# Optimization experiments

Measured on AMD Instinct MI355X. Metric: run time of the kernel, lower is better.

## Reference

```python
import jax, jax.numpy as jnp
import numpy as np

V, C, D = 131072, 65536, 128
E_NEG, E_CON = 131072, 524288
L, B = 3, 32


def setup_inputs() -> dict:
    key = jax.random.key(0)
    ks = jax.random.split(key, 16)
    s = 1.0 / np.sqrt(D)
    return {
        "x_var": jax.random.normal(ks[0], (V, D), jnp.float32),
        "x_con": jax.random.normal(ks[1], (C, D), jnp.float32),
        "W_src": jax.random.normal(ks[2], (L, 3, D, D), jnp.float32) * s,
        "W_dst": jax.random.normal(ks[3], (L, 3, D, D), jnp.float32) * s,
        "att_src": jax.random.normal(ks[4], (L, 3, D), jnp.float32) * s,
        "att_dst": jax.random.normal(ks[5], (L, 3, D), jnp.float32) * s,
        "bias": jnp.zeros((L, 3, D), jnp.float32),
        "mlp_w1": jax.random.normal(ks[6], (D, D), jnp.float32) * s,
        "mlp_b1": jnp.zeros((D,), jnp.float32),
        "mlp_w2": jax.random.normal(ks[7], (D, 1), jnp.float32) * s,
        "mlp_b2": jnp.zeros((1,), jnp.float32),
        "edge_neg_src": jax.random.randint(ks[8], (E_NEG,), 0, V, jnp.int32),
        "edge_neg_dst": jax.random.randint(ks[9], (E_NEG,), 0, V, jnp.int32),
        "edge_con_src": jax.random.randint(ks[10], (E_CON,), 0, V, jnp.int32),
        "edge_con_dst": jax.random.randint(ks[11], (E_CON,), 0, C, jnp.int32),
        "batch_var": jnp.sort(jax.random.randint(ks[12], (V,), 0, B, jnp.int32)),
    }


def _gat(xs, xd, src, dst, Ws, Wd, a_s, a_d, b, n_dst):
    """PyG GATConv (heads=1, add_self_loops=False) for one bipartite relation."""
    hs = xs @ Ws                                    # [Ns, D]
    hd = xd @ Wd                                    # [Nd, D]
    es = hs @ a_s                                   # [Ns]
    ed = hd @ a_d                                   # [Nd]
    e = jax.nn.leaky_relu(es[src] + ed[dst], negative_slope=0.2)  # [E]
    m = jax.ops.segment_max(e, dst, num_segments=n_dst)
    m = jnp.where(jnp.isfinite(m), m, 0.0)
    ex = jnp.exp(e - m[dst])
    den = jax.ops.segment_sum(ex, dst, num_segments=n_dst)
    alpha = ex / (den[dst] + 1e-16)                 # per-destination softmax
    out = jax.ops.segment_sum(hs[src] * alpha[:, None], dst, num_segments=n_dst)
    return out + b


def reference(x_var, x_con, W_src, W_dst, att_src, att_dst, bias,
              mlp_w1, mlp_b1, mlp_w2, mlp_b2,
              edge_neg_src, edge_neg_dst, edge_con_src, edge_con_dst, batch_var):
    xv, xc = x_var, x_con
    n_layers = W_src.shape[0]
    for l in range(n_layers):
        # relation 0: variable -is_negation_of-> variable
        v_neg = _gat(xv, xv, edge_neg_src, edge_neg_dst,
                     W_src[l, 0], W_dst[l, 0], att_src[l, 0], att_dst[l, 0], bias[l, 0], V)
        # relation 2: constraint -rev_connected_to-> variable (reverse edges)
        v_rev = _gat(xc, xv, edge_con_dst, edge_con_src,
                     W_src[l, 2], W_dst[l, 2], att_src[l, 2], att_dst[l, 2], bias[l, 2], V)
        # relation 1: variable -connected_to-> constraint
        c_new = _gat(xv, xc, edge_con_src, edge_con_dst,
                     W_src[l, 1], W_dst[l, 1], att_src[l, 1], att_dst[l, 1], bias[l, 1], C)
        # HeteroConv aggr='sum', then relu (dropout is identity in eval)
        xv = jax.nn.relu(v_neg + v_rev)
        xc = jax.nn.relu(c_new)
    # global_mean_pool over variable nodes per graph
    cnt = jax.ops.segment_sum(jnp.ones((V,), xv.dtype), batch_var, num_segments=B)
    pooled = jax.ops.segment_sum(xv, batch_var, num_segments=B) / jnp.maximum(cnt, 1.0)[:, None]
    # vote MLP: Linear -> relu -> Linear
    h = jax.nn.relu(pooled @ mlp_w1 + mlp_b1)
    return h @ mlp_w2 + mlp_b2
```

## Files before the change

### kernel.cpp

```cpp
#include <hip/hip_runtime.h>
#include <hip/hip_bf16.h>
#include <cstdint>
#include <cstddef>

#define D 128

typedef __hip_bfloat16 bf16;
typedef __attribute__((ext_vector_type(8))) short short8v;
typedef __attribute__((ext_vector_type(4))) float f32x4;

__device__ inline float ld1(const float* p) { return *p; }
__device__ inline float ld1(const bf16* p) { return __bfloat162float(*p); }
__device__ inline float2 ld2(const float* p) { return *(const float2*)p; }
__device__ inline float2 ld2(const bf16* p) {
  __hip_bfloat162 v = *(const __hip_bfloat162*)p;
  float2 r; r.x = __bfloat162float(v.x); r.y = __bfloat162float(v.y); return r;
}
__device__ inline void st2(float* p, float a, float b) {
  float2 v; v.x = a; v.y = b; *(float2*)p = v;
}
__device__ inline void st2(bf16* p, float a, float b) {
  __hip_bfloat162 v; v.x = __float2bfloat16(a); v.y = __float2bfloat16(b);
  *(__hip_bfloat162*)p = v;
}

__device__ inline short f2bf(float x) {
  uint32_t u = __builtin_bit_cast(uint32_t, x);
  uint32_t r = (u + 0x7FFFu + ((u >> 16) & 1u)) >> 16;
  return (short)(uint16_t)r;
}
__device__ inline float bf2f(short s) {
  uint32_t u = ((uint32_t)(uint16_t)s) << 16;
  return __builtin_bit_cast(float, u);
}

__device__ inline f32x4 mfma16(short8v a, short8v b, f32x4 c) {
  return __builtin_amdgcn_mfma_f32_16x16x32_bf16(a, b, c, 0, 0, 0);
}

__device__ __forceinline__ void load8(const float* p, float* v) {
  float4 a = *(const float4*)p;
  float4 b = *(const float4*)(p + 4);
  v[0] = a.x; v[1] = a.y; v[2] = a.z; v[3] = a.w;
  v[4] = b.x; v[5] = b.y; v[6] = b.z; v[7] = b.w;
}

__global__ void compute_u_kernel(const float* __restrict__ Wsrc, const float* __restrict__ Wdst,
                                 const float* __restrict__ asrc, const float* __restrict__ adst,
                                 float* __restrict__ u) {
  int lr = blockIdx.x;
  int side = blockIdx.y;
  int k = threadIdx.x;
  const float* W = (side == 0 ? Wsrc : Wdst) + ((size_t)lr * D + k) * D;
  const float* a = (side == 0 ? asrc : adst) + (size_t)lr * D;
  float s = 0.f;
  for (int j = 0; j < D; ++j) s += W[j] * a[j];
  u[((size_t)lr * 2 + side) * D + k] = s;
}

__global__ void wsplit_kernel(const float* __restrict__ Wsrc,
                              short* __restrict__ WhT, short* __restrict__ WlT) {
  int lr = blockIdx.x;
  const float* W = Wsrc + (size_t)lr * D * D;
  short* wh = WhT + (size_t)lr * D * D;
  short* wl = WlT + (size_t)lr * D * D;
  for (int i = threadIdx.x; i < D * D; i += blockDim.x) {
    int k = i >> 7, c = i & 127;
    float w = W[i];
    short h = f2bf(w);
    short l = f2bf(w - bf2f(h));
    wh[c * D + k] = h;
    wl[c * D + k] = l;
  }
}

__global__ void usplit_kernel(const float* __restrict__ u,
                              short* __restrict__ uh, short* __restrict__ ul, int L) {
  int l = blockIdx.x;
  int j = blockIdx.y;
  int k = threadIdx.x;
  int rel, side;
  switch (j) {
    case 0: rel = 0; side = 0; break;
    case 1: rel = 0; side = 1; break;
    case 2: rel = 1; side = 0; break;
    case 3: rel = 2; side = 1; break;
    case 4: rel = 2; side = 0; break;
    default: rel = 1; side = 1; break;
  }
  float w = u[(((size_t)l * 3 + rel) * 2 + side) * D + k];
  short h = f2bf(w);
  uh[((size_t)l * 6 + j) * D + k] = h;
  ul[((size_t)l * 6 + j) * D + k] = f2bf(w - bf2f(h));
}

__global__ void count_kernel(const int* __restrict__ dst, int* __restrict__ cnt, int E) {
  int i = blockIdx.x * blockDim.x + threadIdx.x;
  if (i < E) atomicAdd(&cnt[dst[i]], 1);
}

__global__ void count2_kernel(const int* __restrict__ csrc, const int* __restrict__ cdst,
                              int* __restrict__ cnt_bycon, int* __restrict__ cnt_byvar, int E) {
  int i = blockIdx.x * blockDim.x + threadIdx.x;
  if (i < E) {
    atomicAdd(&cnt_bycon[cdst[i]], 1);
    atomicAdd(&cnt_byvar[csrc[i]], 1);
  }
}

__global__ void bsum3_kernel(const int* __restrict__ c0, const int* __restrict__ c1,
                             const int* __restrict__ c2, int* __restrict__ bsums,
                             int n0, int n1, int n2, int pb0, int pb1, int pb2) {
  __shared__ int red[256];
  int y = blockIdx.y;
  const int* cnt = (y == 0) ? c0 : (y == 1) ? c1 : c2;
  int n  = (y == 0) ? n0 : (y == 1) ? n1 : n2;
  int pb = (y == 0) ? pb0 : (y == 1) ? pb1 : pb2;
  int b = blockIdx.x, t = threadIdx.x;
  int base = b * pb;
  if (base >= n) return;
  int end = base + pb; if (end > n) end = n;
  int s = 0;
  for (int i = base + t; i < end; i += 256) s += cnt[i];
  red[t] = s;
  __syncthreads();
  #pragma unroll
  for (int off = 128; off; off >>= 1) {
    if (t < off) red[t] += red[t + off];
    __syncthreads();
  }
  if (t == 0) bsums[y * 1024 + b] = red[0];
}

__global__ void bscan3_kernel(int* __restrict__ bsums,
                              int* __restrict__ t0, int* __restrict__ t1, int* __restrict__ t2) {
  __shared__ int sh[1024];
  int y = blockIdx.x, t = threadIdx.x;
  int* bs = bsums + y * 1024;
  int v = bs[t];
  sh[t] = v;
  __syncthreads();
  for (int off = 1; off < 1024; off <<= 1) {
    int u = (t >= off) ? sh[t - off] : 0;
    __syncthreads();
    sh[t] += u;
    __syncthreads();
  }
  bs[t] = sh[t] - v;
  if (t == 1023) {
    int* tot = (y == 0) ? t0 : (y == 1) ? t1 : t2;
    *tot = sh[1023];
  }
}

__global__ void scanfill3_kernel(const int* __restrict__ c0, const int* __restrict__ c1,
                                 const int* __restrict__ c2, const int* __restrict__ bsums,
                                 int* __restrict__ rp0, int* __restrict__ rp1, int* __restrict__ rp2,
                                 int* __restrict__ cu0, int* __restrict__ cu1, int* __restrict__ cu2,
                                 int n0, int n1, int n2, int pb0, int pb1, int pb2) {
  __shared__ int sh[256];
  int y = blockIdx.y;
  const int* cnt = (y == 0) ? c0 : (y == 1) ? c1 : c2;
  int* rowptr    = (y == 0) ? rp0 : (y == 1) ? rp1 : rp2;
  int* cursor    = (y == 0) ? cu0 : (y == 1) ? cu1 : cu2;
  int n  = (y == 0) ? n0 : (y == 1) ? n1 : n2;
  int pb = (y == 0) ? pb0 : (y == 1) ? pb1 : pb2;
  int b = blockIdx.x, t = threadIdx.x;
  int base = b * pb;
  if (base >= n) return;
  int end = base + pb; if (end > n) end = n;
  int run = bsums[y * 1024 + b];
  for (int tile = base; tile < end; tile += 256) {
    int i = tile + t;
    int c = (i < end) ? cnt[i] : 0;
    __syncthreads();
    sh[t] = c;
    __syncthreads();
    for (int off = 1; off < 256; off <<= 1) {
      int u = (t >= off) ? sh[t - off] : 0;
      __syncthreads();
      sh[t] += u;
      __syncthreads();
    }
    int excl = sh[t] - c;
    if (i < end) {
      rowptr[i] = run + excl;
      cursor[i] = run + excl;
    }
    run += sh[255];
  }
}

__global__ void fill_kernel(const int* __restrict__ dst, const int* __restrict__ src,
                            int* __restrict__ cursor, int* __restrict__ col, int E) {
  int i = blockIdx.x * blockDim.x + threadIdx.x;
  if (i < E) {
    int p = atomicAdd(&cursor[dst[i]], 1);
    col[p] = src[i];
  }
}

__global__ void fill2_kernel(const int* __restrict__ csrc, const int* __restrict__ cdst,
                             int* __restrict__ cur_bycon, int* __restrict__ cur_byvar,
                             int* __restrict__ col_bycon, int* __restrict__ col_byvar, int E) {
  int i = blockIdx.x * blockDim.x + threadIdx.x;
  if (i < E) {
    int s = csrc[i], d = cdst[i];
    int p = atomicAdd(&cur_bycon[d], 1);
    col_bycon[p] = s;
    int q = atomicAdd(&cur_byvar[s], 1);
    col_byvar[q] = d;
  }
}

template<typename Tin>
__global__ __launch_bounds__(256) void mm3r_kernel(
    const Tin* __restrict__ Xv, const Tin* __restrict__ Xc,
    const short* __restrict__ wh0, const short* __restrict__ wl0,
    const short* __restrict__ wh1, const short* __restrict__ wl1,
    const short* __restrict__ wh2, const short* __restrict__ wl2,
    const short* __restrict__ uah, const short* __restrict__ ual,
    bf16* __restrict__ H0, bf16* __restrict__ H1, bf16* __restrict__ H2,
    float* __restrict__ es0, float* __restrict__ ed0,
    float* __restrict__ es1, float* __restrict__ ed2,
    float* __restrict__ es2, float* __restrict__ ed1,
    int V, int C, int b0, int b1, int b2) {
  int bid = blockIdx.x;
  const Tin* X; const short* wh; const short* wl; bf16* H;
  int nrows, lb, nblk, nu;
  const short* auh; const short* aul;
  float *o0, *o1, *o2, *o3;
  if (bid < b0) {
    X = Xv; wh = wh0; wl = wl0; H = H0; nrows = V; lb = bid; nblk = b0;
    nu = 4; auh = uah; aul = ual;
    o0 = es0; o1 = ed0; o2 = es1; o3 = ed2;
  } else if (bid < b1) {
    X = Xv; wh = wh1; wl = wl1; H = H1; nrows = V; lb = bid - b0; nblk = b1 - b0;
    nu = 0; auh = nullptr; aul = nullptr; o0 = o1 = o2 = o3 = nullptr;
  } else {
    X = Xc; wh = wh2; wl = wl2; H = H2; nrows = C; lb = bid - b1; nblk = b2 - b1;
    nu = 2; auh = uah + 4 * D; aul = ual + 4 * D;
    o0 = es2; o1 = ed1; o2 = o3 = nullptr;
  }
  int nchunks = (nrows + 15) >> 4;
  int tid = threadIdx.x;
  int cp = tid >> 6, lane = tid & 63;
  int c15 = lane & 15, q = lane >> 4;

  short8v Wh_[2][4], Wl_[2][4];
  #pragma unroll
  for (int t = 0; t < 2; ++t) {
    #pragma unroll
    for (int ks = 0; ks < 4; ++ks) {
      int o = (cp * 32 + t * 16 + c15) * D + ks * 32 + q * 8;
      Wh_[t][ks] = *(const short8v*)&wh[o];
      Wl_[t][ks] = *(const short8v*)&wl[o];
    }
  }
  bool doaug = (cp == 0) && (nu > 0);
  short8v Uh_[4], Ul_[4];
  if (doaug) {
    #pragma unroll
    for (int ks = 0; ks < 4; ++ks) {
      if (c15 < nu) {
        int o = c15 * D + ks * 32 + q * 8;
        Uh_[ks] = *(const short8v*)&auh[o];
        Ul_[ks] = *(const short8v*)&aul[o];
      } else {
        Uh_[ks] = (short8v){0, 0, 0, 0, 0, 0, 0, 0};
        Ul_[ks] = (short8v){0, 0, 0, 0, 0, 0, 0, 0};
      }
    }
  }

  for (int ch = lb; ch < nchunks; ch += nblk) {
    int row = ch * 16 + c15;
    bool valid = row < nrows;
    if (!valid) row = nrows - 1;
    const Tin* xp = X + (size_t)row * D + q * 8;
    f32x4 a0 = (f32x4){0.f, 0.f, 0.f, 0.f};
    f32x4 a1 = (f32x4){0.f, 0.f, 0.f, 0.f};
    f32x4 a2 = (f32x4){0.f, 0.f, 0.f, 0.f};
    if constexpr (sizeof(Tin) == 2) {
      short8v xf[4];
      #pragma unroll
      for (int ks = 0; ks < 4; ++ks)
        xf[ks] = *(const short8v*)((const short*)xp + ks * 32);
      #pragma unroll
      for (int ks = 0; ks < 4; ++ks) {
        a0 = mfma16(Wh_[0][ks], xf[ks], a0);
        a0 = mfma16(Wl_[0][ks], xf[ks], a0);
        a1 = mfma16(Wh_[1][ks], xf[ks], a1);
        a1 = mfma16(Wl_[1][ks], xf[ks], a1);
        if (doaug) {
          a2 = mfma16(Uh_[ks], xf[ks], a2);
          a2 = mfma16(Ul_[ks], xf[ks], a2);
        }
      }
    } else {
      short8v xh[4], xl[4];
      #pragma unroll
      for (int ks = 0; ks < 4; ++ks) {
        float v[8];
        load8((const float*)xp + ks * 32, v);
        #pragma unroll
        for (int j = 0; j < 8; ++j) {
          short hj = f2bf(v[j]);
          xh[ks][j] = hj;
          xl[ks][j] = f2bf(v[j] - bf2f(hj));
        }
      }
      #pragma unroll
      for (int ks = 0; ks < 4; ++ks) {
        a0 = mfma16(Wh_[0][ks], xh[ks], a0);
        a0 = mfma16(Wl_[0][ks], xh[ks], a0);
        a0 = mfma16(Wh_[0][ks], xl[ks], a0);
        a1 = mfma16(Wh_[1][ks], xh[ks], a1);
        a1 = mfma16(Wl_[1][ks], xh[ks], a1);
        a1 = mfma16(Wh_[1][ks], xl[ks], a1);
        if (doaug) {
          a2 = mfma16(Uh_[ks], xh[ks], a2);
          a2 = mfma16(Ul_[ks], xh[ks], a2);
          a2 = mfma16(Uh_[ks], xl[ks], a2);
        }
      }
    }
    if (valid) {
      short4 s0, s1;
      s0.x = f2bf(a0[0]); s0.y = f2bf(a0[1]); s0.z = f2bf(a0[2]); s0.w = f2bf(a0[3]);
      s1.x = f2bf(a1[0]); s1.y = f2bf(a1[1]); s1.z = f2bf(a1[2]); s1.w = f2bf(a1[3]);
      size_t hb = (size_t)row * D + cp * 32 + q * 4;
      *(short4*)((short*)H + hb) = s0;
      *(short4*)((short*)H + hb + 16) = s1;
      if (doaug && q == 0) {
        o0[row] = a2[0];
        o1[row] = a2[1];
        if (nu == 4) { o2[row] = a2[2]; o3[row] = a2[3]; }
      }
    }
  }
}

__device__ __forceinline__ void alpha_rel(const int* __restrict__ rp, const int* __restrict__ col,
                                          const float* __restrict__ es, float edst,
                                          int gw, int lane, int2* __restrict__ edata) {
  int p0 = rp[gw];
  int deg = rp[gw + 1] - p0;
  if (deg <= 0) return;
  if (deg <= 64) {
    int s = 0; float e = -3.0e38f;
    if (lane < deg) {
      s = col[p0 + lane];
      float t = es[s] + edst;
      e = t > 0.f ? t : 0.2f * t;
    }
    float m = e;
    #pragma unroll
    for (int off = 32; off; off >>= 1) m = fmaxf(m, __shfl_xor(m, off));
    float ex = (lane < deg) ? __expf(e - m) : 0.f;
    float den = ex;
    #pragma unroll
    for (int off = 32; off; off >>= 1) den += __shfl_xor(den, off);
    float al = ex / (den + 1e-16f);
    if (lane < deg) {
      int2 v; v.x = s; v.y = __builtin_bit_cast(int, al);
      edata[p0 + lane] = v;
    }
  } else {
    float m = -3.0e38f;
    for (int j = lane; j < deg; j += 64) {
      int s = col[p0 + j];
      float t = es[s] + edst;
      t = t > 0.f ? t : 0.2f * t;
      m = fmaxf(m, t);
    }
    #pragma unroll
    for (int off = 32; off; off >>= 1) m = fmaxf(m, __shfl_xor(m, off));
    float den = 0.f;
    for (int j = lane; j < deg; j += 64) {
      int s = col[p0 + j];
      float t = es[s] + edst;
      t = t > 0.f ? t : 0.2f * t;
      den += __expf(t - m);
    }
    #pragma unroll
    for (int off = 32; off; off >>= 1) den += __shfl_xor(den, off);
    float inv = 1.f / (den + 1e-16f);
    for (int j = lane; j < deg; j += 64) {
      int s = col[p0 + j];
      float t = es[s] + edst;
      t = t > 0.f ? t : 0.2f * t;
      int2 v; v.x = s; v.y = __builtin_bit_cast(int, __expf(t - m) * inv);
      edata[p0 + j] = v;
    }
  }
}

__global__ void alpha_all_kernel(const int* __restrict__ rp0, const int* __restrict__ col0,
                                 const float* __restrict__ es0, const float* __restrict__ ed0,
                                 int2* __restrict__ eda0,
                                 const int* __restrict__ rp2, const int* __restrict__ col2,
                                 const float* __restrict__ es2, const float* __restrict__ ed2,
                                 int2* __restrict__ eda2,
                                 const int* __restrict__ rp1, const int* __restrict__ col1,
                                 const float* __restrict__ es1, const float* __restrict__ ed1,
                                 int2* __restrict__ eda1,
                                 int V, int C) {
  int gw = (int)(((size_t)blockIdx.x * blockDim.x + threadIdx.x) >> 6);
  int lane = threadIdx.x & 63;
  if (gw < V) {
    alpha_rel(rp0, col0, es0, ed0[gw], gw, lane, eda0);
    alpha_rel(rp2, col2, es2, ed2[gw], gw, lane, eda2);
  } else if (gw < V + C) {
    int g = gw - V;
    alpha_rel(rp1, col1, es1, ed1[g], g, lane, eda1);
  }
}

__device__ __forceinline__ void agg_rel(const int2* __restrict__ edata, int p0, int p1,
                                        const bf16* __restrict__ hs, int l2,
                                        float& a0, float& a1) {
  int q = p0;
  while (q + 4 <= p1) {
    int2 e0 = edata[q], e1 = edata[q + 1], e2 = edata[q + 2], e3 = edata[q + 3];
    int s0 = __builtin_amdgcn_readfirstlane(e0.x);
    int s1 = __builtin_amdgcn_readfirstlane(e1.x);
    int s2 = __builtin_amdgcn_readfirstlane(e2.x);
    int s3 = __builtin_amdgcn_readfirstlane(e3.x);
    float w0 = __builtin_bit_cast(float, __builtin_amdgcn_readfirstlane(e0.y));
    float w1 = __builtin_bit_cast(float, __builtin_amdgcn_readfirstlane(e1.y));
    float w2 = __builtin_bit_cast(float, __builtin_amdgcn_readfirstlane(e2.y));
    float w3 = __builtin_bit_cast(float, __builtin_amdgcn_readfirstlane(e3.y));
    float2 h0 = ld2(&hs[(size_t)s0 * D + l2]);
    float2 h1 = ld2(&hs[(size_t)s1 * D + l2]);
    float2 h2 = ld2(&hs[(size_t)s2 * D + l2]);
    float2 h3 = ld2(&hs[(size_t)s3 * D + l2]);
    a0 += w0 * h0.x + w1 * h1.x + w2 * h2.x + w3 * h3.x;
    a1 += w0 * h0.y + w1 * h1.y + w2 * h2.y + w3 * h3.y;
    q += 4;
  }
  while (q < p1) {
    int2 e = edata[q++];
    int s = __builtin_amdgcn_readfirstlane(e.x);
    float w = __builtin_bit_cast(float, __builtin_amdgcn_readfirstlane(e.y));
    float2 h = ld2(&hs[(size_t)s * D + l2]);
    a0 += w * h.x;
    a1 += w * h.y;
  }
}

__global__ void agg_all_kernel(const int* __restrict__ rp0, const int2* __restrict__ eda0,
                               const bf16* __restrict__ hsv0, const float* __restrict__ b0,
                               const int* __restrict__ rp2, const int2* __restrict__ eda2,
                               const bf16* __restrict__ hsc, const float* __restrict__ b2,
                               const int* __restrict__ rp1, const int2* __restrict__ eda1,
                               const bf16* __restrict__ hsv1, const float* __restrict__ b1,
                               bf16* __restrict__ xv_out, bf16* __restrict__ xc_out, int V, int C) {
  int gw = (int)(((size_t)blockIdx.x * blockDim.x + threadIdx.x) >> 6);
  int lane = threadIdx.x & 63;
  int l2 = 2 * lane;
  if (gw < V) {
    float a0 = 0.f, a1 = 0.f;
    agg_rel(eda0, rp0[gw], rp0[gw + 1], hsv0, l2, a0, a1);
    agg_rel(eda2, rp2[gw], rp2[gw + 1], hsc, l2, a0, a1);
    float v0 = a0 + b0[l2] + b2[l2];
    float v1 = a1 + b0[l2 + 1] + b2[l2 + 1];
    st2(&xv_out[(size_t)gw * D + l2], v0 > 0.f ? v0 : 0.f, v1 > 0.f ? v1 : 0.f);
  } else if (gw < V + C) {
    int g = gw - V;
    float a0 = 0.f, a1 = 0.f;
    agg_rel(eda1, rp1[g], rp1[g + 1], hsv1, l2, a0, a1);
    float v0 = a0 + b1[l2];
    float v1 = a1 + b1[l2 + 1];
    st2(&xc_out[(size_t)g * D + l2], v0 > 0.f ? v0 : 0.f, v1 > 0.f ? v1 : 0.f);
  }
}

__global__ void pool_kernel(const bf16* __restrict__ xv, const int* __restrict__ batch,
                            float* __restrict__ pooled, float* __restrict__ cntf,
                            int rowsPerBlock, int V) {
  int j = threadIdx.x;
  int r0 = blockIdx.x * rowsPerBlock;
  if (r0 >= V) return;
  int rend = r0 + rowsPerBlock; if (rend > V) rend = V;
  int cur = batch[r0];
  float s = 0.f;
  int run = 0;
  for (int r = r0; r < rend; ++r) {
    int b = batch[r];
    if (b != cur) {
      atomicAdd(&pooled[(size_t)cur * D + j], s);
      if (j == 0) atomicAdd(&cntf[cur], (float)run);
      s = 0.f; run = 0; cur = b;
    }
    s += ld1(&xv[(size_t)r * D + j]);
    run++;
  }
  atomicAdd(&pooled[(size_t)cur * D + j], s);
  if (j == 0) atomicAdd(&cntf[cur], (float)run);
}

__global__ void mlp_kernel(const float* __restrict__ pooled, const float* __restrict__ cntf,
                           const float* __restrict__ w1, const float* __restrict__ b1,
                           const float* __restrict__ w2, const float* __restrict__ b2,
                           float* __restrict__ out, int B) {
  __shared__ float P[32 * D];
  __shared__ float Hs[32 * D];
  int tid = threadIdx.x;
  if (B > 32) return;
  for (int i = tid; i < B * D; i += 256) {
    int r = i >> 7;
    P[i] = pooled[i] / fmaxf(cntf[r], 1.0f);
  }
  __syncthreads();
  for (int i = tid; i < B * D; i += 256) {
    int r = i >> 7, j = i & 127;
    float s = b1[j];
    for (int k = 0; k < D; ++k) s += P[r * D + k] * w1[k * D + j];
    Hs[i] = s > 0.f ? s : 0.f;
  }
  __syncthreads();
  if (tid < B) {
    float s = b2[0];
    for (int j = 0; j < D; ++j) s += Hs[tid * D + j] * w2[j];
    out[tid] = s;
  }
}

__global__ void zero_kernel(float* __restrict__ o, int n) {
  int i = blockIdx.x * blockDim.x + threadIdx.x;
  if (i < n) o[i] = 0.f;
}

static void run_all(const float* x_var, const float* x_con,
                    const float* W_src, const float* W_dst,
                    const float* att_src, const float* att_dst, const float* bias,
                    const float* mlp_w1, const float* mlp_b1,
                    const float* mlp_w2, const float* mlp_b2,
                    const int* e_neg_src, const int* e_neg_dst,
                    const int* e_con_src, const int* e_con_dst, const int* batch_var,
                    int V, int C, int L, int EN, int EC, int B,
                    char* ws, float* out, hipStream_t stream) {
  size_t off = 0;
  auto alloc = [&](size_t bytes) -> char* {
    char* p = ws + off;
    off = (off + bytes + 255) & ~(size_t)255;
    return p;
  };
  bf16* xv  = (bf16*)alloc((size_t)V * D * 2);
  bf16* xc  = (bf16*)alloc((size_t)C * D * 2);
  bf16* hsv0 = (bf16*)alloc((size_t)V * D * 2);
  bf16* hsv1 = (bf16*)alloc((size_t)V * D * 2);
  bf16* hsc  = (bf16*)alloc((size_t)C * D * 2);
  float* es0 = (float*)alloc((size_t)V * 4);
  float* ed0 = (float*)alloc((size_t)V * 4);
  float* es1 = (float*)alloc((size_t)V * 4);
  float* ed2 = (float*)alloc((size_t)V * 4);
  float* es2 = (float*)alloc((size_t)C * 4);
  float* ed1 = (float*)alloc((size_t)C * 4);
  float* u   = (float*)alloc((size_t)L * 3 * 2 * D * 4);
  short* whT = (short*)alloc((size_t)L * 3 * D * D * 2);
  short* wlT = (short*)alloc((size_t)L * 3 * D * D * 2);
  short* uh  = (short*)alloc((size_t)L * 6 * D * 2);
  short* ul  = (short*)alloc((size_t)L * 6 * D * 2);
  int* rp0  = (int*)alloc((size_t)(V + 1) * 4);
  int* rp1  = (int*)alloc((size_t)(C + 1) * 4);
  int* rp2  = (int*)alloc((size_t)(V + 1) * 4);
  int* curs = (int*)alloc((size_t)(2 * (size_t)V + C) * 4);
  int* cur0 = curs, *cur1 = curs + V, *cur2 = curs + V + C;
  int* col0 = (int*)alloc((size_t)EN * 4);
  int* col1 = (int*)alloc((size_t)EC * 4);
  int* col2 = (int*)alloc((size_t)EC * 4);
  int2* eda0 = (int2*)alloc((size_t)EN * 8);
  int2* eda1 = (int2*)alloc((size_t)EC * 8);
  int2* eda2 = (int2*)alloc((size_t)EC * 8);
  int* bsums = (int*)alloc((size_t)3 * 1024 * 4);
  float* pooled = (float*)alloc((size_t)(B * D + B) * 4);
  float* cntf = pooled + (size_t)B * D;

  hipMemsetAsync(curs, 0, (size_t)(2 * (size_t)V + C) * 4, stream);
  hipMemsetAsync(bsums, 0, (size_t)3 * 1024 * 4, stream);
  hipMemsetAsync(pooled, 0, (size_t)(B * D + B) * 4, stream);

  compute_u_kernel<<<dim3(L * 3, 2), D, 0, stream>>>(W_src, W_dst, att_src, att_dst, u);
  wsplit_kernel<<<L * 3, 256, 0, stream>>>(W_src, whT, wlT);
  usplit_kernel<<<dim3(L, 6), D, 0, stream>>>(u, uh, ul, L);

  const int tb = 256;
  count_kernel<<<(EN + tb - 1) / tb, tb, 0, stream>>>(e_neg_dst, cur0, EN);
  count2_kernel<<<(EC + tb - 1) / tb, tb, 0, stream>>>(e_con_src, e_con_dst, cur1, cur2, EC);

  auto pbof = [](int n) {
    int pb = ((n + 1023) / 1024 + 255) & ~255;
    return pb < 256 ? 256 : pb;
  };
  int pb0 = pbof(V), pb1 = pbof(C), pb2 = pbof(V);
  int nb0 = (V + pb0 - 1) / pb0, nb1 = (C + pb1 - 1) / pb1, nb2 = (V + pb2 - 1) / pb2;
  int nbmax = nb0 > nb1 ? nb0 : nb1; if (nb2 > nbmax) nbmax = nb2;
  bsum3_kernel<<<dim3(nbmax, 3), 256, 0, stream>>>(cur0, cur1, cur2, bsums, V, C, V, pb0, pb1, pb2);
  bscan3_kernel<<<3, 1024, 0, stream>>>(bsums, rp0 + V, rp1 + C, rp2 + V);
  scanfill3_kernel<<<dim3(nbmax, 3), 256, 0, stream>>>(cur0, cur1, cur2, bsums,
                                                       rp0, rp1, rp2, cur0, cur1, cur2,
                                                       V, C, V, pb0, pb1, pb2);

  fill_kernel<<<(EN + tb - 1) / tb, tb, 0, stream>>>(e_neg_dst, e_neg_src, cur0, col0, EN);
  fill2_kernel<<<(EC + tb - 1) / tb, tb, 0, stream>>>(e_con_src, e_con_dst, cur1, cur2, col1, col2, EC);

  auto Wh = [&](int l, int rel) { return whT + ((size_t)l * 3 + rel) * D * D; };
  auto Wl = [&](int l, int rel) { return wlT + ((size_t)l * 3 + rel) * D * D; };
  auto Bp = [&](int l, int rel) { return bias + ((size_t)l * 3 + rel) * D; };

  int gwaves = (V + C + 3) / 4;
  const int MB0 = 1024, MB1 = 2048, MB2 = 2560;

  for (int l = 0; l < L; ++l) {
    const short* uah = uh + (size_t)l * 6 * D;
    const short* ual = ul + (size_t)l * 6 * D;
    if (l == 0) {
      mm3r_kernel<float><<<MB2, 256, 0, stream>>>(
          x_var, x_con, Wh(l,0), Wl(l,0), Wh(l,1), Wl(l,1), Wh(l,2), Wl(l,2),
          uah, ual, hsv0, hsv1, hsc,
          es0, ed0, es1, ed2, es2, ed1, V, C, MB0, MB1, MB2);
    } else {
      mm3r_kernel<bf16><<<MB2, 256, 0, stream>>>(
          xv, xc, Wh(l,0), Wl(l,0), Wh(l,1), Wl(l,1), Wh(l,2), Wl(l,2),
          uah, ual, hsv0, hsv1, hsc,
          es0, ed0, es1, ed2, es2, ed1, V, C, MB0, MB1, MB2);
    }
    alpha_all_kernel<<<gwaves, 256, 0, stream>>>(
        rp0, col0, es0, ed0, eda0,
        rp2, col2, es2, ed2, eda2,
        rp1, col1, es1, ed1, eda1, V, C);
    agg_all_kernel<<<gwaves, 256, 0, stream>>>(
        rp0, eda0, hsv0, Bp(l,0),
        rp2, eda2, hsc,  Bp(l,2),
        rp1, eda1, hsv1, Bp(l,1),
        xv, xc, V, C);
  }

  pool_kernel<<<(V + 127) / 128, 128, 0, stream>>>(xv, batch_var, pooled, cntf, 128, V);
  mlp_kernel<<<1, 256, 0, stream>>>(pooled, cntf, mlp_w1, mlp_b1, mlp_w2, mlp_b2, out, B);
}

extern "C" void kernel_launch(void* const* d_in, const int* in_sizes, int n_in,
                              void* d_out, int out_size, void* d_ws, size_t ws_size,
                              hipStream_t stream) {
  const float* x_var   = (const float*)d_in[0];
  const float* x_con   = (const float*)d_in[1];
  const float* W_src   = (const float*)d_in[2];
  const float* W_dst   = (const float*)d_in[3];
  const float* att_src = (const float*)d_in[4];
  const float* att_dst = (const float*)d_in[5];
  const float* bias    = (const float*)d_in[6];
  const float* mlp_w1  = (const float*)d_in[7];
  const float* mlp_b1  = (const float*)d_in[8];
  const float* mlp_w2  = (const float*)d_in[9];
  const float* mlp_b2  = (const float*)d_in[10];
  const int* e_neg_src = (const int*)d_in[11];
  const int* e_neg_dst = (const int*)d_in[12];
  const int* e_con_src = (const int*)d_in[13];
  const int* e_con_dst = (const int*)d_in[14];
  const int* batch_var = (const int*)d_in[15];
  (void)n_in;

  const int V  = in_sizes[0] / D;
  const int C  = in_sizes[1] / D;
  const int L  = in_sizes[2] / (3 * D * D);
  const int EN = in_sizes[11];
  const int EC = in_sizes[13];
  const int B  = out_size;

  auto plan = [&]() -> size_t {
    size_t o = 0;
    auto add = [&](size_t b) { o = (o + b + 255) & ~(size_t)255; };
    add((size_t)V * D * 2); add((size_t)C * D * 2);
    add((size_t)V * D * 2); add((size_t)V * D * 2); add((size_t)C * D * 2);
    add((size_t)V * 4); add((size_t)V * 4); add((size_t)V * 4); add((size_t)V * 4);
    add((size_t)C * 4); add((size_t)C * 4);
    add((size_t)L * 3 * 2 * D * 4);
    add((size_t)L * 3 * D * D * 2); add((size_t)L * 3 * D * D * 2);
    add((size_t)L * 6 * D * 2); add((size_t)L * 6 * D * 2);
    add((size_t)(V + 1) * 4); add((size_t)(C + 1) * 4); add((size_t)(V + 1) * 4);
    add((size_t)(2 * (size_t)V + C) * 4);
    add((size_t)EN * 4); add((size_t)EC * 4); add((size_t)EC * 4);
    add((size_t)EN * 8); add((size_t)EC * 8); add((size_t)EC * 8);
    add((size_t)3 * 1024 * 4);
    add((size_t)(B * D + B) * 4);
    return o;
  };

  if (plan() <= ws_size) {
    run_all(x_var, x_con, W_src, W_dst, att_src, att_dst, bias,
            mlp_w1, mlp_b1, mlp_w2, mlp_b2,
            e_neg_src, e_neg_dst, e_con_src, e_con_dst, batch_var,
            V, C, L, EN, EC, B, (char*)d_ws, (float*)d_out, stream);
  } else {
    zero_kernel<<<(out_size + 63) / 64, 64, 0, stream>>>((float*)d_out, out_size);
  }
}
```

Before: 974.9 us.

## Split warps into half-warps for wider gathers and prefetch GEMM input rows

The aggregation kernel now has each half-warp process alternate edges, with every lane gathering 4 bf16 features (8 bytes) instead of 2. The two halves are combined with a cross-half shuffle, and the output is written as a short4. This doubles the number of independent gathers in flight per wave and widens each load, targeting the latency-bound random gather of neighbor features. The projection kernel's bf16 path software-prefetches the next chunk's input rows while MFMAs run on the current one, and exits early for idle blocks. f2bf now uses the library conversion, whose NaN handling may differ slightly from the manual rounding.

```diff
diff --git a/kernel.cpp b/kernel.cpp
--- a/kernel.cpp
+++ b/kernel.cpp
@@ -25,9 +25,8 @@
 }
 
 __device__ inline short f2bf(float x) {
-  uint32_t u = __builtin_bit_cast(uint32_t, x);
-  uint32_t r = (u + 0x7FFFu + ((u >> 16) & 1u)) >> 16;
-  return (short)(uint16_t)r;
+  bf16 h = __float2bfloat16(x);
+  return *(short*)&h;
 }
 __device__ inline float bf2f(short s) {
   uint32_t u = ((uint32_t)(uint16_t)s) << 16;
@@ -243,6 +242,7 @@
     o0 = es2; o1 = ed1; o2 = o3 = nullptr;
   }
   int nchunks = (nrows + 15) >> 4;
+  if (lb >= nchunks) return;
   int tid = threadIdx.x;
   int cp = tid >> 6, lane = tid & 63;
   int c15 = lane & 15, q = lane >> 4;
@@ -273,19 +273,29 @@
     }
   }
 
-  for (int ch = lb; ch < nchunks; ch += nblk) {
-    int row = ch * 16 + c15;
-    bool valid = row < nrows;
-    if (!valid) row = nrows - 1;
-    const Tin* xp = X + (size_t)row * D + q * 8;
-    f32x4 a0 = (f32x4){0.f, 0.f, 0.f, 0.f};
-    f32x4 a1 = (f32x4){0.f, 0.f, 0.f, 0.f};
-    f32x4 a2 = (f32x4){0.f, 0.f, 0.f, 0.f};
-    if constexpr (sizeof(Tin) == 2) {
-      short8v xf[4];
+  if constexpr (sizeof(Tin) == 2) {
+    auto xaddr = [&](int ch) -> const short* {
+      int row = ch * 16 + c15;
+      if (row >= nrows) row = nrows - 1;
+      return (const short*)X + (size_t)row * D + q * 8;
+    };
+    short8v xf[4];
+    {
+      const short* xp = xaddr(lb);
       #pragma unroll
-      for (int ks = 0; ks < 4; ++ks)
-        xf[ks] = *(const short8v*)((const short*)xp + ks * 32);
+      for (int ks = 0; ks < 4; ++ks) xf[ks] = *(const short8v*)(xp + ks * 32);
+    }
+    for (int ch = lb; ch < nchunks; ch += nblk) {
+      int nch = ch + nblk;
+      short8v xn[4];
+      if (nch < nchunks) {
+        const short* xp = xaddr(nch);
+        #pragma unroll
+        for (int ks = 0; ks < 4; ++ks) xn[ks] = *(const short8v*)(xp + ks * 32);
+      }
+      f32x4 a0 = (f32x4){0.f, 0.f, 0.f, 0.f};
+      f32x4 a1 = (f32x4){0.f, 0.f, 0.f, 0.f};
+      f32x4 a2 = (f32x4){0.f, 0.f, 0.f, 0.f};
       #pragma unroll
       for (int ks = 0; ks < 4; ++ks) {
         a0 = mfma16(Wh_[0][ks], xf[ks], a0);
@@ -297,7 +307,32 @@
           a2 = mfma16(Ul_[ks], xf[ks], a2);
         }
       }
-    } else {
+      int row = ch * 16 + c15;
+      if (row < nrows) {
+        short4 s0, s1;
+        s0.x = f2bf(a0[0]); s0.y = f2bf(a0[1]); s0.z = f2bf(a0[2]); s0.w = f2bf(a0[3]);
+        s1.x = f2bf(a1[0]); s1.y = f2bf(a1[1]); s1.z = f2bf(a1[2]); s1.w = f2bf(a1[3]);
+        size_t hb = (size_t)row * D + cp * 32 + q * 4;
+        *(short4*)((short*)H + hb) = s0;
+        *(short4*)((short*)H + hb + 16) = s1;
+        if (doaug && q == 0) {
+          o0[row] = a2[0];
+          o1[row] = a2[1];
+          if (nu == 4) { o2[row] = a2[2]; o3[row] = a2[3]; }
+        }
+      }
+      #pragma unroll
+      for (int ks = 0; ks < 4; ++ks) xf[ks] = xn[ks];
+    }
+  } else {
+    for (int ch = lb; ch < nchunks; ch += nblk) {
+      int row = ch * 16 + c15;
+      bool valid = row < nrows;
+      if (!valid) row = nrows - 1;
+      const Tin* xp = X + (size_t)row * D + q * 8;
+      f32x4 a0 = (f32x4){0.f, 0.f, 0.f, 0.f};
+      f32x4 a1 = (f32x4){0.f, 0.f, 0.f, 0.f};
+      f32x4 a2 = (f32x4){0.f, 0.f, 0.f, 0.f};
       short8v xh[4], xl[4];
       #pragma unroll
       for (int ks = 0; ks < 4; ++ks) {
@@ -324,18 +359,18 @@
           a2 = mfma16(Uh_[ks], xl[ks], a2);
         }
       }
-    }
-    if (valid) {
-      short4 s0, s1;
-      s0.x = f2bf(a0[0]); s0.y = f2bf(a0[1]); s0.z = f2bf(a0[2]); s0.w = f2bf(a0[3]);
-      s1.x = f2bf(a1[0]); s1.y = f2bf(a1[1]); s1.z = f2bf(a1[2]); s1.w = f2bf(a1[3]);
-      size_t hb = (size_t)row * D + cp * 32 + q * 4;
-      *(short4*)((short*)H + hb) = s0;
-      *(short4*)((short*)H + hb + 16) = s1;
-      if (doaug && q == 0) {
-        o0[row] = a2[0];
-        o1[row] = a2[1];
-        if (nu == 4) { o2[row] = a2[2]; o3[row] = a2[3]; }
+      if (valid) {
+        short4 s0, s1;
+        s0.x = f2bf(a0[0]); s0.y = f2bf(a0[1]); s0.z = f2bf(a0[2]); s0.w = f2bf(a0[3]);
+        s1.x = f2bf(a1[0]); s1.y = f2bf(a1[1]); s1.z = f2bf(a1[2]); s1.w = f2bf(a1[3]);
+        size_t hb = (size_t)row * D + cp * 32 + q * 4;
+        *(short4*)((short*)H + hb) = s0;
+        *(short4*)((short*)H + hb + 16) = s1;
+        if (doaug && q == 0) {
+          o0[row] = a2[0];
+          o1[row] = a2[1];
+          if (nu == 4) { o2[row] = a2[2]; o3[row] = a2[3]; }
+        }
       }
     }
   }
@@ -417,35 +452,39 @@
   }
 }
 
-__device__ __forceinline__ void agg_rel(const int2* __restrict__ edata, int p0, int p1,
-                                        const bf16* __restrict__ hs, int l2,
-                                        float& a0, float& a1) {
-  int q = p0;
-  while (q + 4 <= p1) {
-    int2 e0 = edata[q], e1 = edata[q + 1], e2 = edata[q + 2], e3 = edata[q + 3];
-    int s0 = __builtin_amdgcn_readfirstlane(e0.x);
-    int s1 = __builtin_amdgcn_readfirstlane(e1.x);
-    int s2 = __builtin_amdgcn_readfirstlane(e2.x);
-    int s3 = __builtin_amdgcn_readfirstlane(e3.x);
-    float w0 = __builtin_bit_cast(float, __builtin_amdgcn_readfirstlane(e0.y));
-    float w1 = __builtin_bit_cast(float, __builtin_amdgcn_readfirstlane(e1.y));
-    float w2 = __builtin_bit_cast(float, __builtin_amdgcn_readfirstlane(e2.y));
-    float w3 = __builtin_bit_cast(float, __builtin_amdgcn_readfirstlane(e3.y));
-    float2 h0 = ld2(&hs[(size_t)s0 * D + l2]);
-    float2 h1 = ld2(&hs[(size_t)s1 * D + l2]);
-    float2 h2 = ld2(&hs[(size_t)s2 * D + l2]);
-    float2 h3 = ld2(&hs[(size_t)s3 * D + l2]);
-    a0 += w0 * h0.x + w1 * h1.x + w2 * h2.x + w3 * h3.x;
-    a1 += w0 * h0.y + w1 * h1.y + w2 * h2.y + w3 * h3.y;
-    q += 4;
+__device__ __forceinline__ void gload4(const bf16* p, float* h) {
+  short4 s = *(const short4*)p;
+  h[0] = bf2f(s.x); h[1] = bf2f(s.y); h[2] = bf2f(s.z); h[3] = bf2f(s.w);
+}
+
+__device__ __forceinline__ void agg_rel2(const int2* __restrict__ edata, int p0, int p1,
+                                         const bf16* __restrict__ hs, int c4, int half,
+                                         float* a) {
+  int q = p0 + half;
+  while (q + 6 < p1) {
+    int2 e0 = edata[q], e1 = edata[q + 2], e2 = edata[q + 4], e3 = edata[q + 6];
+    float h0[4], h1[4], h2[4], h3[4];
+    gload4(&hs[(size_t)e0.x * D + c4], h0);
+    gload4(&hs[(size_t)e1.x * D + c4], h1);
+    gload4(&hs[(size_t)e2.x * D + c4], h2);
+    gload4(&hs[(size_t)e3.x * D + c4], h3);
+    float w0 = __builtin_bit_cast(float, e0.y);
+    float w1 = __builtin_bit_cast(float, e1.y);
+    float w2 = __builtin_bit_cast(float, e2.y);
+    float w3 = __builtin_bit_cast(float, e3.y);
+    #pragma unroll
+    for (int j = 0; j < 4; ++j)
+      a[j] += w0 * h0[j] + w1 * h1[j] + w2 * h2[j] + w3 * h3[j];
+    q += 8;
   }
   while (q < p1) {
-    int2 e = edata[q++];
-    int s = __builtin_amdgcn_readfirstlane(e.x);
-    float w = __builtin_bit_cast(float, __builtin_amdgcn_readfirstlane(e.y));
-    float2 h = ld2(&hs[(size_t)s * D + l2]);
-    a0 += w * h.x;
-    a1 += w * h.y;
+    int2 e = edata[q];
+    float h[4];
+    gload4(&hs[(size_t)e.x * D + c4], h);
+    float w = __builtin_bit_cast(float, e.y);
+    #pragma unroll
+    for (int j = 0; j < 4; ++j) a[j] += w * h[j];
+    q += 2;
   }
 }
 
@@ -458,21 +497,42 @@
                                bf16* __restrict__ xv_out, bf16* __restrict__ xc_out, int V, int C) {
   int gw = (int)(((size_t)blockIdx.x * blockDim.x + threadIdx.x) >> 6);
   int lane = threadIdx.x & 63;
-  int l2 = 2 * lane;
+  int half = lane >> 5;
+  int c4 = (lane & 31) * 4;
+  float a[4] = {0.f, 0.f, 0.f, 0.f};
   if (gw < V) {
-    float a0 = 0.f, a1 = 0.f;
-    agg_rel(eda0, rp0[gw], rp0[gw + 1], hsv0, l2, a0, a1);
-    agg_rel(eda2, rp2[gw], rp2[gw + 1], hsc, l2, a0, a1);
-    float v0 = a0 + b0[l2] + b2[l2];
-    float v1 = a1 + b0[l2 + 1] + b2[l2 + 1];
-    st2(&xv_out[(size_t)gw * D + l2], v0 > 0.f ? v0 : 0.f, v1 > 0.f ? v1 : 0.f);
+    agg_rel2(eda0, rp0[gw], rp0[gw + 1], hsv0, c4, half, a);
+    agg_rel2(eda2, rp2[gw], rp2[gw + 1], hsc, c4, half, a);
+    #pragma unroll
+    for (int j = 0; j < 4; ++j) a[j] += __shfl_xor(a[j], 32);
+    if (half == 0) {
+      float4 ba = *(const float4*)&b0[c4];
+      float4 bb = *(const float4*)&b2[c4];
+      float v0 = a[0] + ba.x + bb.x, v1 = a[1] + ba.y + bb.y;
+      float v2 = a[2] + ba.z + bb.z, v3 = a[3] + ba.w + bb.w;
+      short4 o;
+      o.x = f2bf(v0 > 0.f ? v0 : 0.f);
+      o.y = f2bf(v1 > 0.f ? v1 : 0.f);
+      o.z = f2bf(v2 > 0.f ? v2 : 0.f);
+      o.w = f2bf(v3 > 0.f ? v3 : 0.f);
+      *(short4*)((short*)xv_out + (size_t)gw * D + c4) = o;
+    }
   } else if (gw < V + C) {
     int g = gw - V;
-    float a0 = 0.f, a1 = 0.f;
-    agg_rel(eda1, rp1[g], rp1[g + 1], hsv1, l2, a0, a1);
-    float v0 = a0 + b1[l2];
-    float v1 = a1 + b1[l2 + 1];
-    st2(&xc_out[(size_t)g * D + l2], v0 > 0.f ? v0 : 0.f, v1 > 0.f ? v1 : 0.f);
+    agg_rel2(eda1, rp1[g], rp1[g + 1], hsv1, c4, half, a);
+    #pragma unroll
+    for (int j = 0; j < 4; ++j) a[j] += __shfl_xor(a[j], 32);
+    if (half == 0) {
+      float4 ba = *(const float4*)&b1[c4];
+      float v0 = a[0] + ba.x, v1 = a[1] + ba.y;
+      float v2 = a[2] + ba.z, v3 = a[3] + ba.w;
+      short4 o;
+      o.x = f2bf(v0 > 0.f ? v0 : 0.f);
+      o.y = f2bf(v1 > 0.f ? v1 : 0.f);
+      o.z = f2bf(v2 > 0.f ? v2 : 0.f);
+      o.w = f2bf(v3 > 0.f ? v3 : 0.f);
+      *(short4*)((short*)xc_out + (size_t)g * D + c4) = o;
+    }
   }
 }
 
```

New measurement: 970.4 us. Within noise of the previous version (-0.5%).
